# Kernel tuning notes

Measured on AMD Instinct MI355X. Metric: run time of the kernel, lower is better.

Reference implementation:

```python
import jax, jax.numpy as jnp
import numpy as np

T, H, N, C = 128, 16, 64, 256
S_TGT = 64
S = 2 * S_TGT + 1  # 129, must be >= T (required by original impl's count_computable indexing)
BLANK = 0
TINY = float(np.finfo(np.float32).tiny)
LOG_TINY = float(np.log(TINY))


def _log_add(a, b):
    # faithful to module's log_add: max + log1p(exp(min - max))
    x = jnp.maximum(a, b)
    y = jnp.minimum(a, b)
    return x + jnp.log1p(jnp.exp(y - x))


def _log_sum_h(x):
    # log(max(sum(exp(x), axis=1), tiny));  x: (S,H,N) -> (S,N)
    return jnp.log(jnp.maximum(jnp.sum(jnp.exp(x), axis=1), TINY))


def _expand_with_blank(targets):
    # (N, St) -> (N, 2*St+1): blank-interleaved label sequence
    Nn, St = targets.shape
    blank = jnp.full((Nn, St), BLANK, dtype=targets.dtype)
    et = jnp.stack([blank, targets], axis=-1).reshape(Nn, -1)
    return jnp.concatenate([et, blank[:, :1]], axis=-1)


def _ctc2d_loss(mask, classify, targets, target_lengths):
    Tn, Hn = classify.shape[:2]
    et = _expand_with_blank(targets.astype(jnp.int32))  # (N, S)
    Nn, Ss = et.shape
    dt = classify.dtype

    # alpha init: log(tiny / H) everywhere, rows 0/1 from first frame
    p0 = jnp.full((Ss, Hn, Nn), LOG_TINY - float(np.log(Hn)), dtype=dt)
    p0 = p0.at[0].set(classify[0, :, :, BLANK])
    idx1 = jnp.broadcast_to(et[:, 1][None, :, None], (Hn, Nn, 1))
    p0 = p0.at[1].set(jnp.take_along_axis(classify[0], idx1, axis=2)[..., 0])

    mask_skip = (et[:, 2:] != et[:, :-2]).T  # (S-2, N) bool
    msf = mask_skip.astype(dt)
    # count of computable states, cumulated over "time" (leading dim size S)
    cc = jnp.cumsum(jnp.concatenate([msf[:1] + 1, msf[:1] + 1, msf + 1], axis=0), axis=0)  # (S,N)
    # mask of states not yet reachable at each timestep 1..T-1
    mask_unc = jnp.arange(Ss)[None, :, None] > cc[1:Tn][:, None, :]  # (T-1, S, N)

    et_idx = jnp.broadcast_to(et[None, :, :], (Hn, Nn, Ss))  # gather indices into class dim

    def step(prob, xs):
        m_prev, cls_t, unc = xs  # (H,N), (H,N,C), (S,N)
        hs = _log_sum_h(prob + m_prev[None])          # collapse height: (S,N)
        hs = jnp.where(unc, LOG_TINY, hs)             # zero-out unreachable states
        np1 = _log_add(hs[1:], hs[:-1])               # stay/advance-1: (S-1,N)
        np2 = jnp.where(mask_skip, _log_add(np1[1:], hs[:-2]), np1[1:])  # skip: (S-2,N)
        newp = jnp.concatenate([hs[:1], np1[:1], np2], axis=0)  # (S,N)
        cls_g = jnp.take_along_axis(cls_t, et_idx, axis=2).transpose(2, 0, 1)  # (S,H,N)
        return newp[:, None, :] + cls_g, None

    prob, _ = jax.lax.scan(step, p0, (mask[:Tn - 1], classify[1:], mask_unc))

    # final: sequential log_add over height (faithful to safe_log_sum)
    x = prob + mask[Tn - 1][None]  # (S,H,N)
    res = x[:, 0]
    for i in range(1, Hn):
        res = _log_add(res, x[:, i])  # (S,N)

    lengths = (target_lengths * 2 + 1).astype(jnp.int32)  # (N,)
    g1 = jnp.take_along_axis(res, (lengths - 1)[None, :], axis=0)[0]
    g2 = jnp.take_along_axis(res, (lengths - 2)[None, :], axis=0)[0]
    loss = _log_add(g1, g2)
    return -(loss / target_lengths.astype(dt))  # reduction='mean' per original code


def setup_inputs() -> dict:
    key = jax.random.key(0)
    k0, k1, k2, k3 = jax.random.split(key, 4)
    mask = jax.nn.log_softmax(jax.random.normal(k0, (T, H, N), dtype=jnp.float32), axis=1)
    classify = jax.nn.log_softmax(jax.random.normal(k1, (T, H, N, C), dtype=jnp.float32), axis=3)
    targets = jax.random.randint(k2, (N, S_TGT), 1, C)  # labels cannot be blank
    input_lengths = jnp.full((N,), T, dtype=jnp.int32)
    target_lengths = jax.random.randint(k3, (N,), S_TGT // 2, S_TGT + 1)
    return {"mask": mask, "classify": classify, "targets": targets,
            "input_lengths": input_lengths, "target_lengths": target_lengths}


def reference(mask, classify, targets, input_lengths, target_lengths):
    # input_lengths is accepted but unused, exactly as in the original forward
    return _ctc2d_loss(mask, classify, targets, target_lengths)
```

## Files before the change

kernel.cpp:

```cpp
#include <hip/hip_runtime.h>
#include <math.h>

#define T_DIM 128
#define H_DIM 16
#define N_DIM 64
#define C_DIM 256
#define S_DIM 129
#define LOG_TINY (-87.336544750553109f)

__device__ __forceinline__ float logadd_(float a, float b) {
    float m = fmaxf(a, b);
    float d = fminf(a, b) - m;
    return m + __logf(1.0f + __expf(d));
}

__global__ __launch_bounds__(256) void gc_kernel(
    const float* __restrict__ mask,
    const float* __restrict__ classify,
    float* __restrict__ Gc)
{
    const int b = blockIdx.x;
    const int t = b >> 6;
    const int n = b & 63;
    const int c = threadIdx.x;

    __shared__ float m_lds[H_DIM];
    if (threadIdx.x < H_DIM)
        m_lds[threadIdx.x] = mask[(t * H_DIM + threadIdx.x) * N_DIM + n];
    __syncthreads();

    const float* base = classify + ((size_t)t * H_DIM * N_DIM + n) * C_DIM + c;

    float x[H_DIM];
    float mx = -3.4e38f;
#pragma unroll
    for (int h = 0; h < H_DIM; ++h) {
        x[h] = base[(size_t)h * N_DIM * C_DIM] + m_lds[h];
        mx = fmaxf(mx, x[h]);
    }
    float s = 0.f;
#pragma unroll
    for (int h = 0; h < H_DIM; ++h)
        s += __expf(x[h] - mx);

    Gc[((size_t)t * N_DIM + n) * C_DIM + c] = mx + __logf(s);
}

__global__ __launch_bounds__(192) void scan_kernel(
    const float* __restrict__ Gc,
    const int*   __restrict__ targets,
    const int*   __restrict__ tlen,
    float*       __restrict__ out)
{
    const int n = blockIdx.x;
    const int s = threadIdx.x;

    __shared__ float hsbuf[2][S_DIM + 3];
    __shared__ unsigned char skip_lds[T_DIM - 1];
    __shared__ float resbuf[S_DIM];

    int et = 0;
    if (s < S_DIM && (s & 1)) et = targets[n * 64 + (s >> 1)];

    if (s < T_DIM - 1) {
        int v = 0;
        if (s & 1)
            v = (targets[n * 64 + ((s + 1) >> 1)] !=
                 targets[n * 64 + ((s - 1) >> 1)]) ? 1 : 0;
        skip_lds[s] = (unsigned char)v;
    }
    __syncthreads();

    int skip_s = 0;
    if (s >= 2 && s < S_DIM) skip_s = skip_lds[s - 2];

    float v = (s < 2) ? 0.f : -1e30f;

    const float* gptr = Gc + (size_t)n * C_DIM + et;
    float g = (s < S_DIM) ? gptr[0] : 0.f;

    int cc = 2;

#pragma unroll 1
    for (int i = 0; i < T_DIM - 1; ++i) {
        if (i >= 1) cc += 1 + (int)skip_lds[i - 1];

        float gn = (s < S_DIM) ? gptr[(size_t)(i + 1) * N_DIM * C_DIM] : 0.f;

        float hs = fmaxf(v + g, LOG_TINY);
        if (s > cc) hs = LOG_TINY;

        if (s < S_DIM) hsbuf[i & 1][s] = hs;
        __syncthreads();

        if (s < S_DIM) {
            if (s == 0) {
                v = hs;
            } else {
                float a = logadd_(hs, hsbuf[i & 1][s - 1]);
                if (skip_s) a = logadd_(a, hsbuf[i & 1][s - 2]);
                v = a;
            }
        }
        g = gn;
    }

    if (s < S_DIM) resbuf[s] = v + g;
    __syncthreads();

    if (s == 0) {
        int tl = tlen[n];
        float g1 = resbuf[2 * tl];
        float g2 = resbuf[2 * tl - 1];
        out[n] = -(logadd_(g1, g2) / (float)tl);
    }
}

extern "C" void kernel_launch(void* const* d_in, const int* in_sizes, int n_in,
                              void* d_out, int out_size, void* d_ws, size_t ws_size,
                              hipStream_t stream) {
    const float* mask     = (const float*)d_in[0];
    const float* classify = (const float*)d_in[1];
    const int*   targets  = (const int*)d_in[2];
    const int*   tlen     = (const int*)d_in[4];
    float*       out      = (float*)d_out;

    float* Gc = (float*)d_ws;

    gc_kernel<<<dim3(T_DIM * N_DIM), dim3(256), 0, stream>>>(mask, classify, Gc);
    scan_kernel<<<dim3(N_DIM), dim3(192), 0, stream>>>(Gc, targets, tlen, out);
}
```

Measured before the change: 266.5 us.

## Gather target logsumexp in producer and run CTC scan in a single wavefront

The height-logsumexp kernel now loads float4 vectors, handles four batch items per block, and writes only the values at target and blank classes into a compact per-sample, time-major buffer. The scan kernel loads that buffer into LDS and runs on one 64-lane wavefront, each lane owning three states. Neighbouring states are exchanged with shuffles and the skip mask comes from a ballot, so the per-step __syncthreads is gone. This targets the barrier-bound serial recurrence and the scattered global reads of the full class table, in exchange for more per-lane arithmetic and special-case handling of the last state.

```diff
diff --git a/kernel.cpp b/kernel.cpp
--- a/kernel.cpp
+++ b/kernel.cpp
@@ -17,103 +17,131 @@
 __global__ __launch_bounds__(256) void gc_kernel(
     const float* __restrict__ mask,
     const float* __restrict__ classify,
-    float* __restrict__ Gc)
+    const int*   __restrict__ targets,
+    float* __restrict__ Gt,
+    float* __restrict__ Gb)
 {
-    const int b = blockIdx.x;
-    const int t = b >> 6;
-    const int n = b & 63;
-    const int c = threadIdx.x;
+    const int t  = blockIdx.x;
+    const int ng = blockIdx.y;
+    const int nl = threadIdx.x >> 6;
+    const int cg = threadIdx.x & 63;
+    const int c  = cg * 4;
+    const int n  = ng * 4 + nl;
 
-    __shared__ float m_lds[H_DIM];
-    if (threadIdx.x < H_DIM)
-        m_lds[threadIdx.x] = mask[(t * H_DIM + threadIdx.x) * N_DIM + n];
+    __shared__ float m_lds[H_DIM][4];
+    __shared__ float lse_lds[4][C_DIM];
+
+    if (threadIdx.x < 64) {
+        int h  = threadIdx.x >> 2;
+        int nn = threadIdx.x & 3;
+        m_lds[h][nn] = mask[(t * H_DIM + h) * N_DIM + ng * 4 + nn];
+    }
     __syncthreads();
 
-    const float* base = classify + ((size_t)t * H_DIM * N_DIM + n) * C_DIM + c;
+    const float4* base = (const float4*)(classify +
+        ((size_t)t * H_DIM * N_DIM + n) * C_DIM + c);
+    const size_t hstride = (size_t)N_DIM * C_DIM / 4;
 
-    float x[H_DIM];
-    float mx = -3.4e38f;
+    float4 x[H_DIM];
 #pragma unroll
     for (int h = 0; h < H_DIM; ++h) {
-        x[h] = base[(size_t)h * N_DIM * C_DIM] + m_lds[h];
-        mx = fmaxf(mx, x[h]);
+        float4 v = base[h * hstride];
+        float  m = m_lds[h][nl];
+        x[h] = make_float4(v.x + m, v.y + m, v.z + m, v.w + m);
     }
-    float s = 0.f;
+    float4 mx = make_float4(-3.4e38f, -3.4e38f, -3.4e38f, -3.4e38f);
 #pragma unroll
-    for (int h = 0; h < H_DIM; ++h)
-        s += __expf(x[h] - mx);
+    for (int h = 0; h < H_DIM; ++h) {
+        mx.x = fmaxf(mx.x, x[h].x); mx.y = fmaxf(mx.y, x[h].y);
+        mx.z = fmaxf(mx.z, x[h].z); mx.w = fmaxf(mx.w, x[h].w);
+    }
+    float4 s = make_float4(0.f, 0.f, 0.f, 0.f);
+#pragma unroll
+    for (int h = 0; h < H_DIM; ++h) {
+        s.x += __expf(x[h].x - mx.x); s.y += __expf(x[h].y - mx.y);
+        s.z += __expf(x[h].z - mx.z); s.w += __expf(x[h].w - mx.w);
+    }
+    lse_lds[nl][c + 0] = mx.x + __logf(s.x);
+    lse_lds[nl][c + 1] = mx.y + __logf(s.y);
+    lse_lds[nl][c + 2] = mx.z + __logf(s.z);
+    lse_lds[nl][c + 3] = mx.w + __logf(s.w);
+    __syncthreads();
 
-    Gc[((size_t)t * N_DIM + n) * C_DIM + c] = mx + __logf(s);
+    {
+        int l  = cg;
+        int tv = targets[n * 64 + l];
+        Gt[((size_t)n * T_DIM + t) * 64 + l] = lse_lds[nl][tv];
+        if (l == 0) Gb[n * T_DIM + t] = lse_lds[nl][0];
+    }
 }
 
-__global__ __launch_bounds__(192) void scan_kernel(
-    const float* __restrict__ Gc,
+__global__ __launch_bounds__(64) void scan_kernel(
+    const float* __restrict__ Gt,
+    const float* __restrict__ Gb,
     const int*   __restrict__ targets,
     const int*   __restrict__ tlen,
     float*       __restrict__ out)
 {
     const int n = blockIdx.x;
-    const int s = threadIdx.x;
+    const int l = threadIdx.x;
 
-    __shared__ float hsbuf[2][S_DIM + 3];
-    __shared__ unsigned char skip_lds[T_DIM - 1];
-    __shared__ float resbuf[S_DIM];
+    __shared__ float gt_lds[T_DIM * 64];
+    __shared__ float gb_lds[T_DIM];
 
-    int et = 0;
-    if (s < S_DIM && (s & 1)) et = targets[n * 64 + (s >> 1)];
+    const float* gsrc = Gt + (size_t)n * T_DIM * 64;
+#pragma unroll 8
+    for (int j = l; j < T_DIM * 64; j += 64) gt_lds[j] = gsrc[j];
+    gb_lds[l]      = Gb[n * T_DIM + l];
+    gb_lds[l + 64] = Gb[n * T_DIM + l + 64];
 
-    if (s < T_DIM - 1) {
-        int v = 0;
-        if (s & 1)
-            v = (targets[n * 64 + ((s + 1) >> 1)] !=
-                 targets[n * 64 + ((s - 1) >> 1)]) ? 1 : 0;
-        skip_lds[s] = (unsigned char)v;
-    }
+    int tgt_l = targets[n * 64 + l];
+    int tgt_p = __shfl_up(tgt_l, 1, 64);
+    unsigned long long D = __ballot(l > 0 && tgt_l != tgt_p);
+    const int skip1 = (int)((D >> l) & 1ULL) && (l > 0);
+
     __syncthreads();
 
-    int skip_s = 0;
-    if (s >= 2 && s < S_DIM) skip_s = skip_lds[s - 2];
-
-    float v = (s < 2) ? 0.f : -1e30f;
-
-    const float* gptr = Gc + (size_t)n * C_DIM + et;
-    float g = (s < S_DIM) ? gptr[0] : 0.f;
+    float v0 = (l == 0) ? 0.f : -1e30f;
+    float v1 = (l == 0) ? 0.f : -1e30f;
+    float v2 = -1e30f;
 
     int cc = 2;
 
 #pragma unroll 1
     for (int i = 0; i < T_DIM - 1; ++i) {
-        if (i >= 1) cc += 1 + (int)skip_lds[i - 1];
+        if (i >= 1)
+            cc += 1 + (int)((i & 1) ? 0ULL : ((D >> (i >> 1)) & 1ULL));
 
-        float gn = (s < S_DIM) ? gptr[(size_t)(i + 1) * N_DIM * C_DIM] : 0.f;
+        float gb = gb_lds[i];
+        float gt = gt_lds[i * 64 + l];
 
-        float hs = fmaxf(v + g, LOG_TINY);
-        if (s > cc) hs = LOG_TINY;
+        float hs0 = fmaxf(v0 + gb, LOG_TINY);
+        if (2 * l > cc) hs0 = LOG_TINY;
+        float hs1 = fmaxf(v1 + gt, LOG_TINY);
+        if (2 * l + 1 > cc) hs1 = LOG_TINY;
+        float hs2 = fmaxf(v2 + gb, LOG_TINY);
+        if (128 > cc) hs2 = LOG_TINY;
 
-        if (s < S_DIM) hsbuf[i & 1][s] = hs;
-        __syncthreads();
+        float p1 = __shfl_up(hs1, 1, 64);
 
-        if (s < S_DIM) {
-            if (s == 0) {
-                v = hs;
-            } else {
-                float a = logadd_(hs, hsbuf[i & 1][s - 1]);
-                if (skip_s) a = logadd_(a, hsbuf[i & 1][s - 2]);
-                v = a;
-            }
-        }
-        g = gn;
+        v0 = (l == 0) ? hs0 : logadd_(hs0, p1);
+        float a = logadd_(hs1, hs0);
+        if (skip1) a = logadd_(a, p1);
+        v1 = a;
+        v2 = logadd_(hs2, hs1);
     }
 
-    if (s < S_DIM) resbuf[s] = v + g;
-    __syncthreads();
+    float gb_f = gb_lds[T_DIM - 1];
+    float gt_f = gt_lds[(T_DIM - 1) * 64 + l];
+    float res0 = v0 + gb_f;
+    float res1 = v1 + gt_f;
+    float res2 = v2 + gb_f;
 
-    if (s == 0) {
-        int tl = tlen[n];
-        float g1 = resbuf[2 * tl];
-        float g2 = resbuf[2 * tl - 1];
+    int tl = tlen[n];
+    float g1 = (tl == 64) ? __shfl(res2, 63, 64) : __shfl(res0, tl, 64);
+    float g2 = __shfl(res1, tl - 1, 64);
+    if (l == 0)
         out[n] = -(logadd_(g1, g2) / (float)tl);
-    }
 }
 
 extern "C" void kernel_launch(void* const* d_in, const int* in_sizes, int n_in,
@@ -125,8 +153,9 @@
     const int*   tlen     = (const int*)d_in[4];
     float*       out      = (float*)d_out;
 
-    float* Gc = (float*)d_ws;
+    float* Gt = (float*)d_ws;
+    float* Gb = (float*)((char*)d_ws + (size_t)N_DIM * T_DIM * 64 * 4);
 
-    gc_kernel<<<dim3(T_DIM * N_DIM), dim3(256), 0, stream>>>(mask, classify, Gc);
-    scan_kernel<<<dim3(N_DIM), dim3(192), 0, stream>>>(Gc, targets, tlen, out);
+    gc_kernel<<<dim3(T_DIM, 16), dim3(256), 0, stream>>>(mask, classify, targets, Gt, Gb);
+    scan_kernel<<<dim3(N_DIM), dim3(64), 0, stream>>>(Gt, Gb, targets, tlen, out);
 }
```

After: 242.8 us. -8.9%, faster.
